# Kernel optimization log

Measured on AMD Instinct MI355X. Metric: run time of the kernel, lower is better.

## Reference

```python
import jax, jax.numpy as jnp
import numpy as np
from jax import lax

# SSD300/COCO geometry
B, P, C = 16, 8732, 81
V_CENTER, V_SIZE = 0.1, 0.2        # box coder variances
SCORE_THRESH = 0.05
NMS_THRESH = 0.45
DETS_PER_IMG = 100
PRE_NMS_TOPK = 1000                # fixed-size candidate set for jit-compatible NMS
MIN_SIZE = 0.01                    # remove_small_boxes threshold


def setup_inputs() -> dict:
    key = jax.random.key(0)
    k1, k2, k3, k4, k5 = jax.random.split(key, 5)
    # scale logits so a realistic fraction of softmax scores clears SCORE_THRESH
    pred_logits = jax.random.normal(k1, (B, P, C), jnp.float32) * 2.0
    pred_boxes = jax.random.normal(k2, (B, P, 4), jnp.float32) * 0.5
    # priors in (cx, cy, w, h), normalized coords, positive sizes
    cxcy = jax.random.uniform(k3, (P, 2), jnp.float32, 0.05, 0.95)
    wh = jax.random.uniform(k4, (P, 2), jnp.float32, 0.02, 0.4)
    priors = jnp.concatenate([cxcy, wh], axis=-1)
    target_sizes = jax.random.randint(k5, (B, 2), 480, 1333)  # (h, w) per image
    return {"pred_logits": pred_logits, "pred_boxes": pred_boxes,
            "priors": priors, "target_sizes": target_sizes}


def _decode(rel, priors):
    # SSD box coder: rel = (dx, dy, dw, dh), priors = (cx, cy, w, h) -> xyxy
    cxcy = priors[:, :2] + rel[:, :2] * V_CENTER * priors[:, 2:]
    wh = priors[:, 2:] * jnp.exp(rel[:, 2:] * V_SIZE)
    return jnp.concatenate([cxcy - 0.5 * wh, cxcy + 0.5 * wh], axis=-1)


def _pairwise_iou(b):
    # b: [K, 4] xyxy
    area = (b[:, 2] - b[:, 0]) * (b[:, 3] - b[:, 1])
    lt = jnp.maximum(b[:, None, :2], b[None, :, :2])
    rb = jnp.minimum(b[:, None, 2:], b[None, :, 2:])
    whi = jnp.clip(rb - lt, 0.0)
    inter = whi[..., 0] * whi[..., 1]
    return inter / (area[:, None] + area[None, :] - inter + 1e-9)


def _per_image(logits, rel, priors, size_hw):
    nc1 = C - 1  # foreground classes
    # decode and scale to pixel coords: target_size.flip(0).repeat(2) = [w, h, w, h]
    size_hw = size_hw.astype(jnp.float32)
    whwh = jnp.concatenate([size_hw[::-1], size_hw[::-1]])
    boxes = _decode(rel, priors) * whwh                     # [P, 4]
    scores = jax.nn.softmax(logits, axis=-1)[:, 1:]          # [P, C-1], drop background
    # score threshold + remove_small_boxes, fused as a mask (jit-safe)
    size_ok = ((boxes[:, 2] - boxes[:, 0]) >= MIN_SIZE) & \
              ((boxes[:, 3] - boxes[:, 1]) >= MIN_SIZE)      # [P]
    valid = (scores > SCORE_THRESH) & size_ok[:, None]       # [P, C-1]
    s_flat = jnp.where(valid, scores, -1.0).reshape(-1)      # [P*(C-1)]
    vals, idx = lax.top_k(s_flat, PRE_NMS_TOPK)
    prior_idx = idx // nc1
    labels_k = idx % nc1 + 1                                 # class ids in [1, C)
    boxes_k = boxes[prior_idx]                               # [K, 4]
    vmask = vals > 0.0                                       # real candidates
    # batched_nms via per-class coordinate offset
    max_coord = jnp.max(jnp.where(vmask[:, None], boxes_k, 0.0))
    offs_boxes = boxes_k + (labels_k.astype(jnp.float32) * (max_coord + 1.0))[:, None]
    iou = _pairwise_iou(offs_boxes)                          # [K, K]
    cols = jnp.arange(PRE_NMS_TOPK)

    def body(i, keep):
        suppress = (iou[i] > NMS_THRESH) & keep[i] & (cols > i)
        return keep & ~suppress

    keep = lax.fori_loop(0, PRE_NMS_TOPK, body, vmask)
    kept_scores = jnp.where(keep, vals, -1.0)
    fvals, fidx = lax.top_k(kept_scores, DETS_PER_IMG)
    fvalid = fvals > 0.0
    out_boxes = jnp.where(fvalid[:, None], boxes_k[fidx], 0.0)
    out_scores = jnp.where(fvalid, fvals, 0.0)
    out_labels = jnp.where(fvalid, labels_k[fidx], -1)
    return out_boxes, out_scores, out_labels


def reference(pred_logits, pred_boxes, priors, target_sizes):
    boxes, scores, labels = jax.vmap(_per_image, in_axes=(0, 0, None, 0))(
        pred_logits, pred_boxes, priors, target_sizes)
    # padded, fixed-size equivalent of the per-image list of dicts
    return boxes, scores, labels
```

## Files before the change

kernel.cpp:

```cpp
#include <hip/hip_runtime.h>
#include <math.h>

#pragma clang fp contract(off)

#define NIMG 16
#define NP   8732
#define NCLS 81
#define NFG  80
#define KTOP 1000
#define KPAD 1024
#define DETS 100
#define CAPMAX 166912
#define BASEBITS 0x3D000000u
#define CNT_STRIDE 64
#define TILEB 137
#define NBIN 1280

#define OFF_BOXES  0u
#define OFF_CNT    2235392u
#define OFF_CSCORE 2239488u
#define OFF_CLABEL 2305024u
#define OFF_CBOX   2370560u
#define OFF_COFFS  2632704u
#define OFF_CAREA  2894848u
#define OFF_VALIDW 2960384u
#define OFF_MASK   2962432u
#define OFF_CAND   5059584u

typedef unsigned long long u64;
typedef unsigned int u32;

#define AS_GLOBAL __attribute__((address_space(1)))
#define AS_LOCAL  __attribute__((address_space(3)))

__global__ __launch_bounds__(256, 6) void k_decode(
    const float* __restrict__ logits, const float* __restrict__ rel,
    const float* __restrict__ priors, const int* __restrict__ tsz,
    float* __restrict__ boxes_out, u64* __restrict__ cand,
    u32* __restrict__ cnt, int cap)
{
#pragma clang fp contract(off)
    __shared__ __align__(16) float lx[64 * NCLS];
    __shared__ float pmx[4 * 64];
    __shared__ float psm[4 * 64];
    __shared__ u32 sok[64];
    __shared__ u32 wtt[4];
    __shared__ u32 sbase;
    int b  = blockIdx.x / TILEB;
    int g  = blockIdx.x - b * TILEB;
    int p0 = g * 64;
    int t  = threadIdx.x;
    int lane = t & 63;
    int q = t >> 6;
    int npri = NP - p0; if (npri > 64) npri = 64;
    int words = npri * NCLS;

    const u32* s32 = (const u32*)(logits + ((size_t)b * NP + p0) * NCLS);
    u32* lxw = (u32*)lx;
    int full = words >> 8;
    for (int k = q; k < full; k += 4)
        __builtin_amdgcn_global_load_lds(
            (AS_GLOBAL const u32*)(s32 + (k << 8) + (lane << 2)),
            (AS_LOCAL u32*)(lxw + (k << 8)), 16, 0, 0);
    int base = full << 8;
    int c4 = (words - base) >> 6;
    for (int k = q; k < c4; k += 4)
        __builtin_amdgcn_global_load_lds(
            (AS_GLOBAL const u32*)(s32 + base + (k << 6) + lane),
            (AS_LOCAL u32*)(lxw + base + (k << 6)), 4, 0, 0);
    int base2 = base + (c4 << 6);
    if (q == 0 && lane < words - base2) lxw[base2 + lane] = s32[base2 + lane];

    int p = p0 + lane;
    bool active = p < NP;

    if (q == 0) {
        u32 ok = 0;
        if (active) {
            float4 pr = ((const float4*)priors)[p];
            float4 rl = ((const float4*)rel)[(size_t)b * NP + p];
            float W = (float)tsz[b * 2 + 1], H = (float)tsz[b * 2 + 0];
            float cx = pr.x + (rl.x * 0.1f) * pr.z;
            float cy = pr.y + (rl.y * 0.1f) * pr.w;
            float w_ = pr.z * expf(rl.z * 0.2f);
            float h_ = pr.w * expf(rl.w * 0.2f);
            float4 bx;
            bx.x = (cx - 0.5f * w_) * W; bx.y = (cy - 0.5f * h_) * H;
            bx.z = (cx + 0.5f * w_) * W; bx.w = (cy + 0.5f * h_) * H;
            ((float4*)boxes_out)[(size_t)b * NP + p] = bx;
            ok = ((bx.z - bx.x) >= 0.01f) && ((bx.w - bx.y) >= 0.01f);
        }
        sok[lane] = ok;
    }
    __syncthreads();

    int tb = lane * NCLS;
    int nk = (q == 0) ? 21 : 20;
    float x[21];
    #pragma unroll
    for (int k = 0; k < 21; ++k) {
        int c = q + 4 * k;
        x[k] = (k < nk) ? lx[tb + c] : -3.4e38f;
    }
    float pm = -3.4e38f;
    #pragma unroll
    for (int k = 0; k < 21; ++k) if (k < nk) pm = fmaxf(pm, x[k]);
    pmx[q * 64 + lane] = pm;
    __syncthreads();
    float m = fmaxf(fmaxf(pmx[lane], pmx[64 + lane]),
                    fmaxf(pmx[128 + lane], pmx[192 + lane]));

    float ps = 0.f;
    #pragma unroll
    for (int k = 0; k < 21; ++k) {
        if (k < nk) { x[k] = expf(x[k] - m); ps += x[k]; }
    }
    psm[q * 64 + lane] = ps;
    __syncthreads();
    float s = (psm[lane] + psm[64 + lane]) + (psm[128 + lane] + psm[192 + lane]);

    float hi = 0.05000075f * s;
    float lo = 0.04999925f * s;
    u32 pass = 0, band = 0;
    u32 sizeok = sok[lane];
    if (active && sizeok) {
        #pragma unroll
        for (int k = 0; k < 21; ++k) {
            int c = q + 4 * k;
            if (k < nk && c >= 1) {
                bool pa = x[k] > hi;
                bool bd = (!pa) && (x[k] > lo);
                pass |= ((u32)pa) << k;
                band |= ((u32)bd) << k;
            }
        }
    }
    while (band) {
        int k = __builtin_ctz(band); band &= band - 1;
        int c = q + 4 * k;
        float e = expf(lx[tb + c] - m);
        if (e / s > 0.05f) pass |= 1u << k;
    }
    int cnt_t = __popc(pass);

    int pre = cnt_t;
    #pragma unroll
    for (int d = 1; d < 64; d <<= 1) {
        int o = __shfl_up(pre, d);
        if (lane >= d) pre += o;
    }
    if (lane == 63) wtt[q] = (u32)pre;
    __syncthreads();
    u32 before = 0;
    for (int w = 0; w < 4; ++w) if (w < q) before += wtt[w];
    if (t == 0) {
        u32 tot = wtt[0] + wtt[1] + wtt[2] + wtt[3];
        sbase = tot ? atomicAdd(cnt + b * CNT_STRIDE, tot) : 0u;
    }
    __syncthreads();
    u32 pos = sbase + before + (u32)(pre - cnt_t);

    u64* cb = cand + (size_t)b * cap;
    u32 flatneg = 0xFFFFFFFFu - (u32)p * NFG;
    while (pass) {
        int k = __builtin_ctz(pass); pass &= pass - 1;
        int c = q + 4 * k;
        float e = expf(lx[tb + c] - m);
        float d = e / s;
        if ((int)pos < cap)
            cb[pos] = ((u64)__float_as_uint(d) << 32) | (u64)(flatneg - (u32)(c - 1));
        ++pos;
    }
}

__device__ __forceinline__ void suffix_find(
    u32* hist, u32* wt, u32 K, int tid,
    volatile int* outI, volatile u32* outNext)
{
    int lane = tid & 63, w = tid >> 6;
    u32 v[8]; u32 tot = 0;
    #pragma unroll
    for (int k = 0; k < 8; ++k) { v[k] = hist[tid * 8 + k]; tot += v[k]; }
    u32 ws = tot;
    #pragma unroll
    for (int d = 1; d < 64; d <<= 1) {
        u32 o = __shfl_down(ws, d);
        if (lane + d < 64) ws += o;
    }
    if (lane == 0) wt[w] = ws;
    __syncthreads();
    u32 tail = 0;
    for (int w2 = w + 1; w2 < 16; ++w2) tail += wt[w2];
    u32 after = (ws - tot) + tail;
    u32 sufk[9];
    sufk[8] = after;
    #pragma unroll
    for (int k = 7; k >= 0; --k) sufk[k] = v[k] + sufk[k + 1];
    #pragma unroll
    for (int k = 0; k < 8; ++k) {
        if (sufk[k] >= K && sufk[k + 1] < K) {
            *outI = tid * 8 + k;
            *outNext = sufk[k + 1];
        }
    }
    __syncthreads();
}

__global__ __launch_bounds__(1024) void k_select(
    const u64* __restrict__ cand, const u32* __restrict__ cnt,
    const float* __restrict__ boxes,
    float* __restrict__ cscore, int* __restrict__ clabel,
    float4* __restrict__ cbox, float4* __restrict__ coffs,
    float* __restrict__ carea, u64* __restrict__ validw, int cap)
{
#pragma clang fp contract(off)
    __shared__ u32 h[NBIN];
    __shared__ u32 fh[8192];
    __shared__ u32 wt[16];
    __shared__ u64 buf[2048];
    __shared__ float red16[16];
    __shared__ int sh_c, sh_i2;
    __shared__ u32 sh_S, sh_next, sh_d, sh_m;
    int b = blockIdx.x, t = threadIdx.x, lane = t & 63;
    u32 n = min(cnt[b * CNT_STRIDE], (u32)cap);
    const u64* cb = cand + (size_t)b * cap;

    for (int i = t; i < NBIN; i += 1024) h[i] = 0;
    if (t == 0) { sh_c = -2; sh_i2 = -2; sh_S = 0; sh_next = 0; sh_m = 0; }
    __syncthreads();
    if (t == 0 && (n & 1)) {
        u32 sb = (u32)(cb[n - 1] >> 32);
        u32 bin = (sb - BASEBITS) >> 15; if (bin > NBIN - 1) bin = NBIN - 1;
        atomicAdd(&h[bin], 1u);
    }
    u32 npair = n >> 1;
    for (u32 bs0 = 0; bs0 < npair; bs0 += 4096) {
        u32 i0 = bs0 + (u32)t;
        uint4 va, vb, vc, vd;
        bool q0 = i0 < npair, q1 = i0 + 1024 < npair,
             q2 = i0 + 2048 < npair, q3 = i0 + 3072 < npair;
        if (q0) va = ((const uint4*)cb)[i0];
        if (q1) vb = ((const uint4*)cb)[i0 + 1024];
        if (q2) vc = ((const uint4*)cb)[i0 + 2048];
        if (q3) vd = ((const uint4*)cb)[i0 + 3072];
        if (q0) {
            u32 b1 = (va.y - BASEBITS) >> 15; if (b1 > NBIN - 1) b1 = NBIN - 1;
            u32 b2 = (va.w - BASEBITS) >> 15; if (b2 > NBIN - 1) b2 = NBIN - 1;
            atomicAdd(&h[b1], 1u); atomicAdd(&h[b2], 1u);
        }
        if (q1) {
            u32 b1 = (vb.y - BASEBITS) >> 15; if (b1 > NBIN - 1) b1 = NBIN - 1;
            u32 b2 = (vb.w - BASEBITS) >> 15; if (b2 > NBIN - 1) b2 = NBIN - 1;
            atomicAdd(&h[b1], 1u); atomicAdd(&h[b2], 1u);
        }
        if (q2) {
            u32 b1 = (vc.y - BASEBITS) >> 15; if (b1 > NBIN - 1) b1 = NBIN - 1;
            u32 b2 = (vc.w - BASEBITS) >> 15; if (b2 > NBIN - 1) b2 = NBIN - 1;
            atomicAdd(&h[b1], 1u); atomicAdd(&h[b2], 1u);
        }
        if (q3) {
            u32 b1 = (vd.y - BASEBITS) >> 15; if (b1 > NBIN - 1) b1 = NBIN - 1;
            u32 b2 = (vd.w - BASEBITS) >> 15; if (b2 > NBIN - 1) b2 = NBIN - 1;
            atomicAdd(&h[b1], 1u); atomicAdd(&h[b2], 1u);
        }
    }
    __syncthreads();
    if (t < 64) {
        u32 v[20]; u32 tot = 0;
        #pragma unroll
        for (int k = 0; k < 20; ++k) { v[k] = h[t * 20 + k]; tot += v[k]; }
        u32 ws = tot;
        #pragma unroll
        for (int d = 1; d < 64; d <<= 1) {
            u32 o = (u32)__shfl_down((int)ws, d);
            if (t + d < 64) ws += o;
        }
        u32 suf[21];
        suf[20] = ws - tot;
        #pragma unroll
        for (int k = 19; k >= 0; --k) suf[k] = v[k] + suf[k + 1];
        #pragma unroll
        for (int k = 0; k < 20; ++k) {
            if (suf[k] >= (u32)KTOP && suf[k + 1] < (u32)KTOP) {
                sh_c = t * 20 + k; sh_S = suf[k]; sh_next = suf[k + 1];
            }
        }
    }
    __syncthreads();
    int c = sh_c;
    u32 T = 0;
    if (c >= 0) {
        if (sh_S <= 2048u) {
            T = BASEBITS + ((u32)c << 15);
        } else {
            u32 nhi = sh_next;
            for (int i = t; i < 8192; i += 1024) fh[i] = 0;
            __syncthreads();
            for (u32 i = (u32)t; i < n; i += 1024) {
                u32 sb = (u32)(cb[i] >> 32);
                if ((int)((sb - BASEBITS) >> 15) == c)
                    atomicAdd(&fh[(sb >> 2) & 0x1FFFu], 1u);
            }
            __syncthreads();
            suffix_find(fh, wt, (u32)KTOP - nhi, t, &sh_i2, &sh_d);
            T = (sh_i2 >= 0) ? (BASEBITS + ((u32)c << 15) + ((u32)sh_i2 << 2))
                             : (BASEBITS + ((u32)c << 15));
        }
    }
    for (u32 bs0 = 0; bs0 < n; bs0 += 4096) {
        u32 i0 = bs0 + (u32)t;
        u64 k0 = 0, k1 = 0, k2 = 0, k3 = 0;
        bool q0 = i0 < n, q1 = i0 + 1024 < n, q2 = i0 + 2048 < n, q3 = i0 + 3072 < n;
        if (q0) k0 = cb[i0];
        if (q1) k1 = cb[i0 + 1024];
        if (q2) k2 = cb[i0 + 2048];
        if (q3) k3 = cb[i0 + 3072];
        #pragma unroll
        for (int e = 0; e < 4; ++e) {
            u64 key = (e == 0) ? k0 : (e == 1) ? k1 : (e == 2) ? k2 : k3;
            bool pr = (e == 0) ? q0 : (e == 1) ? q1 : (e == 2) ? q2 : q3;
            bool pick = pr && ((u32)(key >> 32) >= T);
            u64 bal = __ballot(pick);
            u32 wb = 0;
            if (lane == 0 && bal) wb = atomicAdd(&sh_m, (u32)__popcll(bal));
            wb = (u32)__shfl((int)wb, 0);
            if (pick) {
                u32 pos = wb + (u32)__popcll(bal & ((1ULL << lane) - 1ULL));
                if (pos < 2048) buf[pos] = key;
            }
        }
    }
    __syncthreads();
    u32 m = min(sh_m, 2048u);
    for (int i = t; i < 2048; i += 1024) if ((u32)i >= m) buf[i] = 0ULL;
    __syncthreads();
    for (int k = 2; k <= 2048; k <<= 1) {
        for (int j = k >> 1; j >= 64; j >>= 1) {
            #pragma unroll
            for (int e = 0; e < 2; ++e) {
                int i = t + e * 1024;
                int ixj = i ^ j;
                if (ixj > i) {
                    u64 a = buf[i], bb = buf[ixj];
                    bool up = (i & k) == 0;
                    if (up ? (a < bb) : (a > bb)) { buf[i] = bb; buf[ixj] = a; }
                }
            }
            __syncthreads();
        }
        u64 v0 = buf[t], v1 = buf[t + 1024];
        bool up0 = (t & k) == 0;
        bool up1 = ((t + 1024) & k) == 0;
        int js = ((k >> 1) < 32) ? (k >> 1) : 32;
        for (int j = js; j >= 1; j >>= 1) {
            u64 o0 = __shfl_xor(v0, j);
            u64 o1 = __shfl_xor(v1, j);
            bool lo0 = (t & j) == 0;
            v0 = (lo0 == up0) ? (v0 > o0 ? v0 : o0) : (v0 < o0 ? v0 : o0);
            v1 = (lo0 == up1) ? (v1 > o1 ? v1 : o1) : (v1 < o1 ? v1 : o1);
        }
        buf[t] = v0; buf[t + 1024] = v1;
        __syncthreads();
    }
    u64 key = (t < KTOP) ? buf[t] : 0ULL;
    float s = __uint_as_float((u32)(key >> 32));
    bool valid = s > 0.0f;
    u32 flat = valid ? (0xFFFFFFFFu - (u32)key) : 0u;
    int prior = (int)(flat / NFG);
    int cls = (int)(flat - (u32)prior * NFG) + 1;
    float4 bx = make_float4(0.f, 0.f, 0.f, 0.f);
    if (valid) bx = ((const float4*)boxes)[b * NP + prior];
    cscore[b * KPAD + t] = s;
    clabel[b * KPAD + t] = cls;
    cbox[b * KPAD + t] = bx;
    u64 vb = __ballot(valid);
    if (lane == 0) validw[b * 16 + (t >> 6)] = vb;
    float lm = valid ? fmaxf(fmaxf(bx.x, bx.y), fmaxf(bx.z, bx.w)) : 0.0f;
    lm = fmaxf(lm, 0.0f);
    #pragma unroll
    for (int d = 1; d < 64; d <<= 1) lm = fmaxf(lm, __shfl_xor(lm, d));
    if (lane == 0) red16[t >> 6] = lm;
    __syncthreads();
    float mc = red16[0];
    #pragma unroll
    for (int w = 1; w < 16; ++w) mc = fmaxf(mc, red16[w]);
    float off = (float)cls * (mc + 1.0f);
    float4 ob = valid ? make_float4(bx.x + off, bx.y + off, bx.z + off, bx.w + off)
                      : make_float4(0.f, 0.f, 0.f, 0.f);
    float area = valid ? (ob.z - ob.x) * (ob.w - ob.y) : 0.0f;
    coffs[b * KPAD + t] = ob;
    carea[b * KPAD + t] = area;
}

__global__ __launch_bounds__(1024) void k_iou(
    const float4* __restrict__ coffs, const float* __restrict__ carea,
    u64* __restrict__ cmask)
{
#pragma clang fp contract(off)
    __shared__ float4 bs[KPAD];
    __shared__ float as_[KPAD];
    int b = blockIdx.x >> 4, tile = blockIdx.x & 15;
    int t = threadIdx.x;
    bs[t] = coffs[b * KPAD + t];
    as_[t] = carea[b * KPAD + t];
    __syncthreads();
    int j = tile * 64 + (t & 63);
    int w = t >> 6;
    float4 bj = bs[j];
    float aj = as_[j];
    int r0 = w * 64;
    u64 bits = 0;
    #pragma unroll 4
    for (int k = 0; k < 64; ++k) {
        int r = r0 + k;
        float4 br = bs[r];
        float ar = as_[r];
        float ltx = fmaxf(br.x, bj.x), lty = fmaxf(br.y, bj.y);
        float rbx = fminf(br.z, bj.z), rby = fminf(br.w, bj.w);
        float wx = fmaxf(rbx - ltx, 0.0f), wy = fmaxf(rby - lty, 0.0f);
        float inter = wx * wy;
        float denom = ((ar + aj) - inter) + 1e-9f;
        float iou = inter / denom;
        bool sup = (iou > 0.45f) && (j > r);
        bits |= ((u64)sup) << k;
    }
    cmask[((size_t)b * 16 + w) * KPAD + j] = bits;
}

__global__ __launch_bounds__(64) void k_nms(
    const u64* __restrict__ cmask, const u64* __restrict__ validw,
    const float* __restrict__ cscore, const int* __restrict__ clabel,
    const float4* __restrict__ cbox, float* __restrict__ out)
{
    int b = blockIdx.x, lane = threadIdx.x;
    const u64* cm = cmask + (size_t)b * 16 * KPAD;
    u64 kept[16];
    u64 cw[16];
    #pragma unroll
    for (int w = 0; w < 16; ++w) cw[w] = cm[w * KPAD + lane];
    #pragma unroll
    for (int g = 0; g < 16; ++g) {
        u64 vg = validw[b * 16 + g];
        bool rem = false;
        #pragma unroll
        for (int w = 0; w < 16; ++w)
            if (w < g) rem |= (kept[w] & cw[w]) != 0ULL;
        u64 cg = cw[g];
        bool myv = ((vg >> lane) & 1ULL) && !rem;
        if (g < 15) {
            int cbase = (g + 1) * 64 + lane;
            #pragma unroll
            for (int w = 0; w < 16; ++w) cw[w] = cm[w * KPAD + cbase];
        }
        u64 K = __ballot(myv);
        for (;;) {
            u64 K2 = __ballot(myv && ((K & cg) == 0ULL));
            if (K2 == K) break;
            K = K2;
        }
        kept[g] = K;
    }
    __shared__ u64 sk[16];
    __shared__ int pfx[17];
    __shared__ int slot[DETS];
    if (lane == 0) {
        #pragma unroll
        for (int w = 0; w < 16; ++w) sk[w] = kept[w];
        int run = 0;
        #pragma unroll
        for (int l = 0; l < 16; ++l) { pfx[l] = run; run += __popcll(kept[l]); }
        pfx[16] = run;
    }
    __syncthreads();
    if (lane < 16) {
        int r = pfx[lane];
        u64 wv = sk[lane];
        while (wv && r < DETS) {
            int bit = __builtin_ctzll(wv);
            slot[r] = lane * 64 + bit;
            ++r;
            wv &= wv - 1;
        }
    }
    __syncthreads();
    int total = min(pfx[16], DETS);
    for (int r = lane; r < DETS; r += 64) {
        float4 bx = make_float4(0.f, 0.f, 0.f, 0.f);
        float s = 0.0f;
        int lb = -1;
        if (r < total) {
            int cdx = slot[r];
            bx = cbox[b * KPAD + cdx];
            s = cscore[b * KPAD + cdx];
            lb = clabel[b * KPAD + cdx];
        }
        float* ob = out + ((size_t)b * DETS + r) * 4;
        ob[0] = bx.x; ob[1] = bx.y; ob[2] = bx.z; ob[3] = bx.w;
        out[NIMG * DETS * 4 + b * DETS + r] = s;
        out[NIMG * DETS * 4 + NIMG * DETS + b * DETS + r] = (float)lb;
    }
}

extern "C" void kernel_launch(void* const* d_in, const int* in_sizes, int n_in,
                              void* d_out, int out_size, void* d_ws, size_t ws_size,
                              hipStream_t stream) {
    const float* logits = (const float*)d_in[0];
    const float* rel    = (const float*)d_in[1];
    const float* priors = (const float*)d_in[2];
    const int*   tsz    = (const int*)d_in[3];
    float* out = (float*)d_out;
    char* ws = (char*)d_ws;

    float* boxes  = (float*)(ws + OFF_BOXES);
    u32*   cnt    = (u32*)(ws + OFF_CNT);
    float* cscore = (float*)(ws + OFF_CSCORE);
    int*   clabel = (int*)(ws + OFF_CLABEL);
    float4* cbox  = (float4*)(ws + OFF_CBOX);
    float4* coffs = (float4*)(ws + OFF_COFFS);
    float* carea  = (float*)(ws + OFF_CAREA);
    u64*   validw = (u64*)(ws + OFF_VALIDW);
    u64*   cmask  = (u64*)(ws + OFF_MASK);
    u64*   cand   = (u64*)(ws + OFF_CAND);

    long long avail = ((long long)ws_size - (long long)OFF_CAND) / (NIMG * 8);
    int cap = (int)(avail < CAPMAX ? (avail > 0 ? avail : 1) : CAPMAX);
    cap &= ~1;

    hipMemsetAsync(cnt, 0, NIMG * CNT_STRIDE * 4, stream);
    k_decode<<<NIMG * TILEB, 256, 0, stream>>>(logits, rel, priors, tsz,
                                               boxes, cand, cnt, cap);
    k_select<<<NIMG, 1024, 0, stream>>>(cand, cnt, boxes, cscore, clabel,
                                        cbox, coffs, carea, validw, cap);
    k_iou<<<NIMG * 16, 1024, 0, stream>>>(coffs, carea, cmask);
    k_nms<<<NIMG, 64, 0, stream>>>(cmask, validw, cscore, clabel, cbox, out);
}
```

Before: 161.0 us.

## Replace single-pass 1280-bin histogram with two-level privatized radix histogram

Top-K threshold selection now uses a coarse 64-bin histogram followed by a second 64-bin refinement pass restricted to the winning coarse bin, instead of one 1280-bin histogram. Each bin is replicated across 32 columns indexed by lane, which spreads shared-memory atomics and cuts contention on hot bins. The cost is a second full read of the candidate list and an extra reduction and sync stage. The final fine-histogram pass now matches on the combined two-level prefix.

```diff
diff --git a/kernel.cpp b/kernel.cpp
--- a/kernel.cpp
+++ b/kernel.cpp
@@ -14,7 +14,6 @@
 #define BASEBITS 0x3D000000u
 #define CNT_STRIDE 64
 #define TILEB 137
-#define NBIN 1280
 
 #define OFF_BOXES  0u
 #define OFF_CNT    2235392u
@@ -214,24 +213,27 @@
     float* __restrict__ carea, u64* __restrict__ validw, int cap)
 {
 #pragma clang fp contract(off)
-    __shared__ u32 h[NBIN];
+    __shared__ u32 h1[64 * 32];
+    __shared__ u32 h2[64 * 32];
     __shared__ u32 fh[8192];
     __shared__ u32 wt[16];
     __shared__ u64 buf[2048];
     __shared__ float red16[16];
-    __shared__ int sh_c, sh_i2;
-    __shared__ u32 sh_S, sh_next, sh_d, sh_m;
-    int b = blockIdx.x, t = threadIdx.x, lane = t & 63;
+    __shared__ int sh_c1, sh_c2, sh_i2;
+    __shared__ u32 sh_n1hi, sh_S, sh_n2hi, sh_d, sh_m;
+    int b = blockIdx.x, t = threadIdx.x, lane = t & 63, col = t & 31;
     u32 n = min(cnt[b * CNT_STRIDE], (u32)cap);
     const u64* cb = cand + (size_t)b * cap;
 
-    for (int i = t; i < NBIN; i += 1024) h[i] = 0;
-    if (t == 0) { sh_c = -2; sh_i2 = -2; sh_S = 0; sh_next = 0; sh_m = 0; }
-    __syncthreads();
+    for (int i = t; i < 64 * 32; i += 1024) { h1[i] = 0; h2[i] = 0; }
+    if (t == 0) { sh_c1 = -2; sh_c2 = -2; sh_i2 = -2;
+                  sh_n1hi = 0; sh_S = 0; sh_n2hi = 0; sh_m = 0; }
+    __syncthreads();
+
     if (t == 0 && (n & 1)) {
         u32 sb = (u32)(cb[n - 1] >> 32);
-        u32 bin = (sb - BASEBITS) >> 15; if (bin > NBIN - 1) bin = NBIN - 1;
-        atomicAdd(&h[bin], 1u);
+        u32 bb = (sb - BASEBITS) >> 21; if (bb > 63u) bb = 63u;
+        atomicAdd(&h1[bb * 32], 1u);
     }
     u32 npair = n >> 1;
     for (u32 bs0 = 0; bs0 < npair; bs0 += 4096) {
@@ -243,68 +245,92 @@
         if (q1) vb = ((const uint4*)cb)[i0 + 1024];
         if (q2) vc = ((const uint4*)cb)[i0 + 2048];
         if (q3) vd = ((const uint4*)cb)[i0 + 3072];
-        if (q0) {
-            u32 b1 = (va.y - BASEBITS) >> 15; if (b1 > NBIN - 1) b1 = NBIN - 1;
-            u32 b2 = (va.w - BASEBITS) >> 15; if (b2 > NBIN - 1) b2 = NBIN - 1;
-            atomicAdd(&h[b1], 1u); atomicAdd(&h[b2], 1u);
-        }
-        if (q1) {
-            u32 b1 = (vb.y - BASEBITS) >> 15; if (b1 > NBIN - 1) b1 = NBIN - 1;
-            u32 b2 = (vb.w - BASEBITS) >> 15; if (b2 > NBIN - 1) b2 = NBIN - 1;
-            atomicAdd(&h[b1], 1u); atomicAdd(&h[b2], 1u);
-        }
-        if (q2) {
-            u32 b1 = (vc.y - BASEBITS) >> 15; if (b1 > NBIN - 1) b1 = NBIN - 1;
-            u32 b2 = (vc.w - BASEBITS) >> 15; if (b2 > NBIN - 1) b2 = NBIN - 1;
-            atomicAdd(&h[b1], 1u); atomicAdd(&h[b2], 1u);
-        }
-        if (q3) {
-            u32 b1 = (vd.y - BASEBITS) >> 15; if (b1 > NBIN - 1) b1 = NBIN - 1;
-            u32 b2 = (vd.w - BASEBITS) >> 15; if (b2 > NBIN - 1) b2 = NBIN - 1;
-            atomicAdd(&h[b1], 1u); atomicAdd(&h[b2], 1u);
+        u32 sbv[8]; int nv = 0;
+        if (q0) { sbv[nv++] = va.y; sbv[nv++] = va.w; }
+        if (q1) { sbv[nv++] = vb.y; sbv[nv++] = vb.w; }
+        if (q2) { sbv[nv++] = vc.y; sbv[nv++] = vc.w; }
+        if (q3) { sbv[nv++] = vd.y; sbv[nv++] = vd.w; }
+        for (int e = 0; e < nv; ++e) {
+            u32 bb = (sbv[e] - BASEBITS) >> 21; if (bb > 63u) bb = 63u;
+            atomicAdd(&h1[bb * 32 + col], 1u);
         }
     }
     __syncthreads();
     if (t < 64) {
-        u32 v[20]; u32 tot = 0;
-        #pragma unroll
-        for (int k = 0; k < 20; ++k) { v[k] = h[t * 20 + k]; tot += v[k]; }
-        u32 ws = tot;
+        u32 v = 0;
+        #pragma unroll
+        for (int k = 0; k < 32; ++k) v += h1[t * 32 + ((k + t) & 31)];
+        u32 ws = v;
         #pragma unroll
         for (int d = 1; d < 64; d <<= 1) {
             u32 o = (u32)__shfl_down((int)ws, d);
             if (t + d < 64) ws += o;
         }
-        u32 suf[21];
-        suf[20] = ws - tot;
-        #pragma unroll
-        for (int k = 19; k >= 0; --k) suf[k] = v[k] + suf[k + 1];
-        #pragma unroll
-        for (int k = 0; k < 20; ++k) {
-            if (suf[k] >= (u32)KTOP && suf[k + 1] < (u32)KTOP) {
-                sh_c = t * 20 + k; sh_S = suf[k]; sh_next = suf[k + 1];
-            }
-        }
-    }
-    __syncthreads();
-    int c = sh_c;
+        if (ws >= (u32)KTOP && (ws - v) < (u32)KTOP) { sh_c1 = t; sh_n1hi = ws - v; }
+    }
+    __syncthreads();
+    int c1 = sh_c1;
     u32 T = 0;
-    if (c >= 0) {
+    if (c1 >= 0) {
+        u32 n1hi = sh_n1hi;
+        if (t == 0 && (n & 1)) {
+            u32 sb = (u32)(cb[n - 1] >> 32);
+            u32 bb = (sb - BASEBITS) >> 21; if (bb > 63u) bb = 63u;
+            if ((int)bb == c1) atomicAdd(&h2[((sb >> 15) & 63u) * 32], 1u);
+        }
+        for (u32 bs0 = 0; bs0 < npair; bs0 += 4096) {
+            u32 i0 = bs0 + (u32)t;
+            uint4 va, vb, vc, vd;
+            bool q0 = i0 < npair, q1 = i0 + 1024 < npair,
+                 q2 = i0 + 2048 < npair, q3 = i0 + 3072 < npair;
+            if (q0) va = ((const uint4*)cb)[i0];
+            if (q1) vb = ((const uint4*)cb)[i0 + 1024];
+            if (q2) vc = ((const uint4*)cb)[i0 + 2048];
+            if (q3) vd = ((const uint4*)cb)[i0 + 3072];
+            u32 sbv[8]; int nv = 0;
+            if (q0) { sbv[nv++] = va.y; sbv[nv++] = va.w; }
+            if (q1) { sbv[nv++] = vb.y; sbv[nv++] = vb.w; }
+            if (q2) { sbv[nv++] = vc.y; sbv[nv++] = vc.w; }
+            if (q3) { sbv[nv++] = vd.y; sbv[nv++] = vd.w; }
+            for (int e = 0; e < nv; ++e) {
+                u32 bb = (sbv[e] - BASEBITS) >> 21; if (bb > 63u) bb = 63u;
+                if ((int)bb == c1)
+                    atomicAdd(&h2[((sbv[e] >> 15) & 63u) * 32 + col], 1u);
+            }
+        }
+        __syncthreads();
+        if (t < 64) {
+            u32 v = 0;
+            #pragma unroll
+            for (int k = 0; k < 32; ++k) v += h2[t * 32 + ((k + t) & 31)];
+            u32 ws = v;
+            #pragma unroll
+            for (int d = 1; d < 64; d <<= 1) {
+                u32 o = (u32)__shfl_down((int)ws, d);
+                if (t + d < 64) ws += o;
+            }
+            u32 K2 = (u32)KTOP - n1hi;
+            if (ws >= K2 && (ws - v) < K2) {
+                sh_c2 = t; sh_S = n1hi + ws; sh_n2hi = n1hi + (ws - v);
+            }
+        }
+        __syncthreads();
+        int c2 = sh_c2;
+        u32 Tc = BASEBITS + ((u32)c1 << 21) + ((u32)c2 << 15);
         if (sh_S <= 2048u) {
-            T = BASEBITS + ((u32)c << 15);
+            T = Tc;
         } else {
-            u32 nhi = sh_next;
+            u32 nhi = sh_n2hi;
             for (int i = t; i < 8192; i += 1024) fh[i] = 0;
             __syncthreads();
             for (u32 i = (u32)t; i < n; i += 1024) {
                 u32 sb = (u32)(cb[i] >> 32);
-                if ((int)((sb - BASEBITS) >> 15) == c)
+                if ((sb & 0xFFFF8000u) == Tc)
                     atomicAdd(&fh[(sb >> 2) & 0x1FFFu], 1u);
             }
             __syncthreads();
             suffix_find(fh, wt, (u32)KTOP - nhi, t, &sh_i2, &sh_d);
-            T = (sh_i2 >= 0) ? (BASEBITS + ((u32)c << 15) + ((u32)sh_i2 << 2))
-                             : (BASEBITS + ((u32)c << 15));
+            T = (sh_i2 >= 0) ? (Tc + ((u32)sh_i2 << 2)) : Tc;
         }
     }
     for (u32 bs0 = 0; bs0 < n; bs0 += 4096) {
```

After: 173.5 us. 1.08x slower.

## Build score histogram in decode kernel instead of rescanning candidates in select

Applied to the files above, without the earlier changes.

The coarse score histogram used for top-K threshold selection is now built during candidate emission in k_decode. Each block keeps a shared-memory histogram and flushes it to a per-image global histogram with atomics. k_select then loads the finished histogram instead of re-reading the whole candidate buffer, which removes a full pass over up to ~100k+ candidates per image in a kernel that has only 16 blocks. To keep this cheap, the bins become coarser (640 bins of 16 mantissa bits) and the refinement histogram is shifted to match. The cost is extra shared and global atomics in the decode kernel and a larger memset.

```diff
diff --git a/kernel.cpp b/kernel.cpp
--- a/kernel.cpp
+++ b/kernel.cpp
@@ -14,18 +14,20 @@
 #define BASEBITS 0x3D000000u
 #define CNT_STRIDE 64
 #define TILEB 137
-#define NBIN 1280
+#define NB 640
 
 #define OFF_BOXES  0u
 #define OFF_CNT    2235392u
-#define OFF_CSCORE 2239488u
-#define OFF_CLABEL 2305024u
-#define OFF_CBOX   2370560u
-#define OFF_COFFS  2632704u
-#define OFF_CAREA  2894848u
-#define OFF_VALIDW 2960384u
-#define OFF_MASK   2962432u
-#define OFF_CAND   5059584u
+#define OFF_GHIST  2239488u
+#define OFF_CSCORE 2280448u
+#define OFF_CLABEL 2345984u
+#define OFF_CBOX   2411520u
+#define OFF_COFFS  2673664u
+#define OFF_CAREA  2935808u
+#define OFF_VALIDW 3001344u
+#define OFF_MASK   3003392u
+#define OFF_CAND   5100544u
+#define MEMSET_LEN 45056u
 
 typedef unsigned long long u64;
 typedef unsigned int u32;
@@ -37,7 +39,7 @@
     const float* __restrict__ logits, const float* __restrict__ rel,
     const float* __restrict__ priors, const int* __restrict__ tsz,
     float* __restrict__ boxes_out, u64* __restrict__ cand,
-    u32* __restrict__ cnt, int cap)
+    u32* __restrict__ cnt, u32* __restrict__ ghist, int cap)
 {
 #pragma clang fp contract(off)
     __shared__ __align__(16) float lx[64 * NCLS];
@@ -46,6 +48,7 @@
     __shared__ u32 sok[64];
     __shared__ u32 wtt[4];
     __shared__ u32 sbase;
+    __shared__ u32 lhist[NB];
     int b  = blockIdx.x / TILEB;
     int g  = blockIdx.x - b * TILEB;
     int p0 = g * 64;
@@ -71,6 +74,8 @@
     int base2 = base + (c4 << 6);
     if (q == 0 && lane < words - base2) lxw[base2 + lane] = s32[base2 + lane];
 
+    for (int i = t; i < NB; i += 256) lhist[i] = 0;
+
     int p = p0 + lane;
     bool active = p < NP;
 
@@ -167,9 +172,19 @@
         int c = q + 4 * k;
         float e = expf(lx[tb + c] - m);
         float d = e / s;
-        if ((int)pos < cap)
-            cb[pos] = ((u64)__float_as_uint(d) << 32) | (u64)(flatneg - (u32)(c - 1));
+        if ((int)pos < cap) {
+            u32 sb = __float_as_uint(d);
+            cb[pos] = ((u64)sb << 32) | (u64)(flatneg - (u32)(c - 1));
+            u32 bin = (sb - BASEBITS) >> 16; if (bin > NB - 1) bin = NB - 1;
+            atomicAdd(&lhist[bin], 1u);
+        }
         ++pos;
+    }
+    __syncthreads();
+    u32* gh = ghist + b * NB;
+    for (int i = t; i < NB; i += 256) {
+        u32 v = lhist[i];
+        if (v) atomicAdd(gh + i, v);
     }
 }
 
@@ -208,13 +223,13 @@
 
 __global__ __launch_bounds__(1024) void k_select(
     const u64* __restrict__ cand, const u32* __restrict__ cnt,
-    const float* __restrict__ boxes,
+    const u32* __restrict__ ghist, const float* __restrict__ boxes,
     float* __restrict__ cscore, int* __restrict__ clabel,
     float4* __restrict__ cbox, float4* __restrict__ coffs,
     float* __restrict__ carea, u64* __restrict__ validw, int cap)
 {
 #pragma clang fp contract(off)
-    __shared__ u32 h[NBIN];
+    __shared__ u32 h[NB];
     __shared__ u32 fh[8192];
     __shared__ u32 wt[16];
     __shared__ u64 buf[2048];
@@ -225,64 +240,27 @@
     u32 n = min(cnt[b * CNT_STRIDE], (u32)cap);
     const u64* cb = cand + (size_t)b * cap;
 
-    for (int i = t; i < NBIN; i += 1024) h[i] = 0;
+    for (int i = t; i < NB; i += 1024) h[i] = ghist[b * NB + i];
     if (t == 0) { sh_c = -2; sh_i2 = -2; sh_S = 0; sh_next = 0; sh_m = 0; }
     __syncthreads();
-    if (t == 0 && (n & 1)) {
-        u32 sb = (u32)(cb[n - 1] >> 32);
-        u32 bin = (sb - BASEBITS) >> 15; if (bin > NBIN - 1) bin = NBIN - 1;
-        atomicAdd(&h[bin], 1u);
-    }
-    u32 npair = n >> 1;
-    for (u32 bs0 = 0; bs0 < npair; bs0 += 4096) {
-        u32 i0 = bs0 + (u32)t;
-        uint4 va, vb, vc, vd;
-        bool q0 = i0 < npair, q1 = i0 + 1024 < npair,
-             q2 = i0 + 2048 < npair, q3 = i0 + 3072 < npair;
-        if (q0) va = ((const uint4*)cb)[i0];
-        if (q1) vb = ((const uint4*)cb)[i0 + 1024];
-        if (q2) vc = ((const uint4*)cb)[i0 + 2048];
-        if (q3) vd = ((const uint4*)cb)[i0 + 3072];
-        if (q0) {
-            u32 b1 = (va.y - BASEBITS) >> 15; if (b1 > NBIN - 1) b1 = NBIN - 1;
-            u32 b2 = (va.w - BASEBITS) >> 15; if (b2 > NBIN - 1) b2 = NBIN - 1;
-            atomicAdd(&h[b1], 1u); atomicAdd(&h[b2], 1u);
-        }
-        if (q1) {
-            u32 b1 = (vb.y - BASEBITS) >> 15; if (b1 > NBIN - 1) b1 = NBIN - 1;
-            u32 b2 = (vb.w - BASEBITS) >> 15; if (b2 > NBIN - 1) b2 = NBIN - 1;
-            atomicAdd(&h[b1], 1u); atomicAdd(&h[b2], 1u);
-        }
-        if (q2) {
-            u32 b1 = (vc.y - BASEBITS) >> 15; if (b1 > NBIN - 1) b1 = NBIN - 1;
-            u32 b2 = (vc.w - BASEBITS) >> 15; if (b2 > NBIN - 1) b2 = NBIN - 1;
-            atomicAdd(&h[b1], 1u); atomicAdd(&h[b2], 1u);
-        }
-        if (q3) {
-            u32 b1 = (vd.y - BASEBITS) >> 15; if (b1 > NBIN - 1) b1 = NBIN - 1;
-            u32 b2 = (vd.w - BASEBITS) >> 15; if (b2 > NBIN - 1) b2 = NBIN - 1;
-            atomicAdd(&h[b1], 1u); atomicAdd(&h[b2], 1u);
-        }
-    }
-    __syncthreads();
     if (t < 64) {
-        u32 v[20]; u32 tot = 0;
-        #pragma unroll
-        for (int k = 0; k < 20; ++k) { v[k] = h[t * 20 + k]; tot += v[k]; }
+        u32 v[10]; u32 tot = 0;
+        #pragma unroll
+        for (int k = 0; k < 10; ++k) { v[k] = h[t * 10 + k]; tot += v[k]; }
         u32 ws = tot;
         #pragma unroll
         for (int d = 1; d < 64; d <<= 1) {
             u32 o = (u32)__shfl_down((int)ws, d);
             if (t + d < 64) ws += o;
         }
-        u32 suf[21];
-        suf[20] = ws - tot;
-        #pragma unroll
-        for (int k = 19; k >= 0; --k) suf[k] = v[k] + suf[k + 1];
-        #pragma unroll
-        for (int k = 0; k < 20; ++k) {
+        u32 suf[11];
+        suf[10] = ws - tot;
+        #pragma unroll
+        for (int k = 9; k >= 0; --k) suf[k] = v[k] + suf[k + 1];
+        #pragma unroll
+        for (int k = 0; k < 10; ++k) {
             if (suf[k] >= (u32)KTOP && suf[k + 1] < (u32)KTOP) {
-                sh_c = t * 20 + k; sh_S = suf[k]; sh_next = suf[k + 1];
+                sh_c = t * 10 + k; sh_S = suf[k]; sh_next = suf[k + 1];
             }
         }
     }
@@ -290,21 +268,21 @@
     int c = sh_c;
     u32 T = 0;
     if (c >= 0) {
+        u32 Tc = BASEBITS + ((u32)c << 16);
         if (sh_S <= 2048u) {
-            T = BASEBITS + ((u32)c << 15);
+            T = Tc;
         } else {
             u32 nhi = sh_next;
             for (int i = t; i < 8192; i += 1024) fh[i] = 0;
             __syncthreads();
             for (u32 i = (u32)t; i < n; i += 1024) {
                 u32 sb = (u32)(cb[i] >> 32);
-                if ((int)((sb - BASEBITS) >> 15) == c)
-                    atomicAdd(&fh[(sb >> 2) & 0x1FFFu], 1u);
+                if ((sb & 0xFFFF0000u) == Tc)
+                    atomicAdd(&fh[(sb >> 3) & 0x1FFFu], 1u);
             }
             __syncthreads();
             suffix_find(fh, wt, (u32)KTOP - nhi, t, &sh_i2, &sh_d);
-            T = (sh_i2 >= 0) ? (BASEBITS + ((u32)c << 15) + ((u32)sh_i2 << 2))
-                             : (BASEBITS + ((u32)c << 15));
+            T = (sh_i2 >= 0) ? (Tc + ((u32)sh_i2 << 3)) : Tc;
         }
     }
     for (u32 bs0 = 0; bs0 < n; bs0 += 4096) {
@@ -513,6 +491,7 @@
 
     float* boxes  = (float*)(ws + OFF_BOXES);
     u32*   cnt    = (u32*)(ws + OFF_CNT);
+    u32*   ghist  = (u32*)(ws + OFF_GHIST);
     float* cscore = (float*)(ws + OFF_CSCORE);
     int*   clabel = (int*)(ws + OFF_CLABEL);
     float4* cbox  = (float4*)(ws + OFF_CBOX);
@@ -526,10 +505,10 @@
     int cap = (int)(avail < CAPMAX ? (avail > 0 ? avail : 1) : CAPMAX);
     cap &= ~1;
 
-    hipMemsetAsync(cnt, 0, NIMG * CNT_STRIDE * 4, stream);
+    hipMemsetAsync(cnt, 0, MEMSET_LEN, stream);
     k_decode<<<NIMG * TILEB, 256, 0, stream>>>(logits, rel, priors, tsz,
-                                               boxes, cand, cnt, cap);
-    k_select<<<NIMG, 1024, 0, stream>>>(cand, cnt, boxes, cscore, clabel,
+                                               boxes, cand, cnt, ghist, cap);
+    k_select<<<NIMG, 1024, 0, stream>>>(cand, cnt, ghist, boxes, cscore, clabel,
                                         cbox, coffs, carea, validw, cap);
     k_iou<<<NIMG * 16, 1024, 0, stream>>>(coffs, carea, cmask);
     k_nms<<<NIMG, 64, 0, stream>>>(cmask, validw, cscore, clabel, cbox, out);
```

Measured after the change: 157.1 us. -2.4%, faster.
